# Performance work log

Measured on AMD Instinct MI355X. Metric: run time of the kernel, lower is better.

Reference implementation:

```python
import jax, jax.numpy as jnp
import numpy as np
import math
from jax import lax

STRIDES = (8.0, 16.0, 32.0)
ANCHORS = (
    ((6.1, 8.1), (20.6, 12.6), (11.2, 23.7)),
    ((36.2, 26.8), (25.9, 57.2), (57.8, 47.9)),
    ((122.1, 78.3), (73.7, 143.8), (236.1, 213.1)),
)
NUM_CLASSES = 80
L = NUM_CLASSES + 5
NA = 3
SCORE_T = 0.1
NMS_T = 0.6
DETECTIONS = 100
TOPK = 1000          # static cap on post-threshold candidates per image
IMG = 640            # batched image H=W; also max_size used for class offsets


def setup_inputs() -> dict:
    key = jax.random.key(0)
    ks = jax.random.split(key, 8)
    N = 8
    chans = (128, 256, 512)
    hw = (80, 40, 20)
    inp = {}
    for i, (c, s) in enumerate(zip(chans, hw)):
        inp[f"f{i}"] = jax.random.normal(ks[i], (N, c, s, s), jnp.float32)
        inp[f"w{i}"] = jax.random.normal(ks[3 + i], (NA * L, c), jnp.float32) * 0.02
        b = np.zeros((NA, L), np.float32)
        b[:, 4] += math.log(8 / (416 / STRIDES[i]) ** 2)   # Predictor bias init
        b[:, 5:] += math.log(0.6 / (NUM_CLASSES - 0.99))
        inp[f"b{i}"] = jnp.asarray(b.reshape(-1))
    inp["scale_factors"] = jnp.ones((N,), jnp.float32)
    return inp


def _decode_level(f, w, b, stride, anchors):
    # f: [N,Cin,H,W]; w: [NA*L,Cin]; 1x1 conv == channel GEMM
    N, _, H, W = f.shape
    p = jnp.einsum('nchw,oc->nhwo', f, w) + b
    p = jax.nn.sigmoid(p.reshape(N, H, W, NA, L))
    gx, gy = jnp.meshgrid(jnp.arange(W, dtype=f.dtype), jnp.arange(H, dtype=f.dtype), indexing='xy')
    grid = jnp.stack((gx, gy), axis=-1)                       # [H,W,2] (x,y)
    xy = (2 * p[..., :2] - 0.5 + grid[None, :, :, None, :]) * stride
    wh = 4 * p[..., 2:4] ** 2 * anchors[None, None, None, :, :]
    box = jnp.concatenate((xy, wh), axis=-1).reshape(N, -1, 4)
    obj = p[..., 4].reshape(N, -1)
    cls = p[..., 5:].reshape(N, -1, NUM_CLASSES)
    return box, obj, cls


def _cxcywh2xyxy(b):
    cx, cy, w, h = b[..., 0], b[..., 1], b[..., 2], b[..., 3]
    return jnp.stack((cx - w / 2, cy - h / 2, cx + w / 2, cy + h / 2), axis=-1)


def _iou_one_many(b, boxes):
    lt = jnp.maximum(b[:2], boxes[:, :2])
    rb = jnp.minimum(b[2:], boxes[:, 2:])
    wh = jnp.clip(rb - lt, 0)
    inter = wh[:, 0] * wh[:, 1]
    area_b = (b[2] - b[0]) * (b[3] - b[1])
    areas = (boxes[:, 2] - boxes[:, 0]) * (boxes[:, 3] - boxes[:, 1])
    return inter / (area_b + areas - inter + 1e-7)


def _nms_fixed(boxes, scores):
    # greedy NMS, fixed DETECTIONS iterations; boxes already class-offset
    def step(valid, _):
        s = jnp.where(valid, scores, -jnp.inf)
        i = jnp.argmax(s)
        ok = s[i] > 0.0
        ious = _iou_one_many(boxes[i], boxes)
        nv = valid & (ious <= NMS_T)
        nv = nv.at[i].set(False)
        valid = jnp.where(ok, nv, valid)
        return valid, (jnp.where(ok, i, -1), ok)

    valid0 = scores > SCORE_T
    _, (idx, ok) = lax.scan(step, valid0, None, length=DETECTIONS)
    return idx, ok


def _per_image(boxes, obj, cls, sf):
    scores = obj[:, None] * cls                               # [A,C]
    mask = (obj[:, None] > SCORE_T) & (scores > SCORE_T)
    scores = jnp.where(mask, scores, -1.0)
    topv, topi = lax.top_k(scores.reshape(-1), TOPK)
    anchor = topi // NUM_CLASSES
    label = topi % NUM_CLASSES
    cb = boxes[anchor]
    cb = jnp.clip(cb, 0.0, float(IMG))                        # image_shapes = (IMG, IMG)
    off = cb + (label * IMG).astype(cb.dtype)[:, None]        # batched_nms class offset
    idx, ok = _nms_fixed(off, topv)
    gi = jnp.clip(idx, 0)
    okf = ok.astype(cb.dtype)
    out_box = cb[gi] / sf * okf[:, None]
    out_score = topv[gi] * okf
    out_label = label[gi].astype(cb.dtype) * okf
    return jnp.concatenate((out_box, out_score[:, None], out_label[:, None]), axis=1)  # [DET,6]


def reference(f0, f1, f2, w0, b0, w1, b1, w2, b2, scale_factors):
    feats = (f0, f1, f2)
    ws = (w0, w1, w2)
    bs = (b0, b1, b2)
    boxes, objs, clss = [], [], []
    for i in range(3):
        a = jnp.asarray(ANCHORS[i], dtype=f0.dtype)
        bx, ob, cl = _decode_level(feats[i], ws[i], bs[i], STRIDES[i], a)
        boxes.append(bx)
        objs.append(ob)
        clss.append(cl)
    boxes = _cxcywh2xyxy(jnp.concatenate(boxes, axis=1))      # [N, 25200, 4]
    obj = jnp.concatenate(objs, axis=1)                       # [N, 25200]
    cls = jnp.concatenate(clss, axis=1)                       # [N, 25200, 80]
    return jax.vmap(_per_image)(boxes, obj, cls, scale_factors)  # [N, DET, 6]
```

## Files before the change

kernel.cpp:

```cpp
#include <hip/hip_runtime.h>
#include <math.h>


#define NUM_CLASSES 80
#define IMG_F 640.0f

#define LOGITS_F 0
#define N_LOGITS 48000
#define WPACK_F  48000
#define N_WPACK  3584
#define WT_F     (WPACK_F + N_WPACK)
#define N_WT     344064
#define WT_L0    0
#define WT_L1    49152
#define WT_L2    147456
#define CAND_F   (WT_F + N_WT)
#define CAP1     4096
#define CNT_F    (CAND_F + CAP1*2)
#define IMGBUF_F (CNT_F + 16)
#define CAP2     2048

#define LOGIT_T (-2.1972245773362196f)

__constant__ float d_anch[3][3][2] = {
  {{6.1f,8.1f},{20.6f,12.6f},{11.2f,23.7f}},
  {{36.2f,26.8f},{25.9f,57.2f},{57.8f,47.9f}},
  {{122.1f,78.3f},{73.7f,143.8f},{236.1f,213.1f}},
};
__constant__ float d_stridec[3] = {8.f,16.f,32.f};

__global__ __launch_bounds__(256) void k0_init(
    float* __restrict__ ws, float* __restrict__ out,
    const float* __restrict__ w0, const float* __restrict__ w1,
    const float* __restrict__ w2) {
  int i = blockIdx.x * 256 + threadIdx.x;
  if (i < N_LOGITS) ws[LOGITS_F + i] = 0.f;
  if (i < 4800)     out[i] = 0.f;
  if (i < 16)       ((int*)ws)[CNT_F + i] = 0;
  if (i < N_WPACK) {
    int a = i & 3, c4 = i >> 2;
    float v = 0.f;
    if (a < 3) {
      if (c4 < 128)       v = w0[(a*85+4)*128 + c4];
      else if (c4 < 384)  v = w1[(a*85+4)*256 + (c4-128)];
      else                v = w2[(a*85+4)*512 + (c4-384)];
    }
    ws[WPACK_F + i] = v;
  }
  if (i < N_WT) {
    int level, C, i2;
    const float* w;
    if (i < WT_L1)          { level = 0; C = 128; i2 = i;            w = w0; }
    else if (i < WT_L2)     { level = 1; C = 256; i2 = i - WT_L1;    w = w1; }
    else                    { level = 2; C = 512; i2 = i - WT_L2;    w = w2; }
    int a = i2 / (C * 128);
    int r = i2 - a * (C * 128);
    int c = r >> 7, l = r & 127;
    ws[WT_F + i] = (l < 85) ? w[(size_t)(a * 85 + l) * C + c] : 0.f;
    (void)level;
  }
}

__global__ __launch_bounds__(256) void k1_obj(
    const float* __restrict__ f0, const float* __restrict__ f1,
    const float* __restrict__ f2, const float* __restrict__ b0,
    float* __restrict__ ws) {
  __shared__ float4 wl[128];
  int b = blockIdx.x, tid = threadIdx.x;
  int level, posblk, kc;
  if (b < 200)      { level = 0; posblk = b; kc = 0; }
  else if (b < 400) { int t = b - 200; level = 1; posblk = t % 50; kc = t / 50; }
  else              { int t = b - 400; level = 2; posblk = t % 13; kc = t / 13; }
  const int Cs[3]   = {128, 256, 512};
  const int HWs[3]  = {6400, 1600, 400};
  const int KBs[3]  = {1, 4, 8};
  const int W4B[3]  = {0, 128, 384};
  int C = Cs[level], HW = HWs[level], KB = KBs[level];
  int chunk = C / KB;
  const float* f = (level == 0) ? f0 : (level == 1) ? f1 : f2;
  const float4* wp4 = (const float4*)(ws + WPACK_F);
  int c0 = kc * chunk;
  if (tid < chunk) wl[tid] = wp4[W4B[level] + c0 + tid];
  __syncthreads();
  int pos = posblk * 256 + tid;
  if (pos >= 8 * HW) return;
  int n = pos / HW, s = pos - n * HW;
  const float* fp = f + ((size_t)(n * C + c0)) * HW + s;
  float acc[3] = {0.f, 0.f, 0.f};
  #pragma unroll 16
  for (int c = 0; c < chunk; ++c) {
    float fv = fp[(size_t)c * HW];
    float4 w4 = wl[c];
    acc[0] = fmaf(fv, w4.x, acc[0]);
    acc[1] = fmaf(fv, w4.y, acc[1]);
    acc[2] = fmaf(fv, w4.z, acc[2]);
  }
  if (level == 0) {
    #pragma unroll
    for (int a = 0; a < 3; ++a) {
      float logit = acc[a] + b0[a * 85 + 4];
      if (logit > LOGIT_T) {
        float obj = 1.f / (1.f + expf(-logit));
        int idx = atomicAdd((int*)ws + CNT_F, 1);
        if (idx < CAP1) {
          int* cd = (int*)ws + CAND_F + idx * 2;
          cd[0] = (n << 24) | (0 << 20) | (a << 16) | s;
          ((float*)cd)[1] = obj;
        }
      }
    }
  } else {
    float* lg = ws + LOGITS_F + n * 6000 + ((level == 1) ? 0 : 4800) + s * 3;
    atomicAdd(lg + 0, acc[0]);
    atomicAdd(lg + 1, acc[1]);
    atomicAdd(lg + 2, acc[2]);
  }
}

__global__ __launch_bounds__(256) void k1b_thresh(
    float* __restrict__ ws, const float* __restrict__ b1,
    const float* __restrict__ b2) {
  int i = blockIdx.x * 256 + threadIdx.x;
  if (i >= N_LOGITS) return;
  int n = i / 6000, r = i - n * 6000;
  int level = (r < 4800) ? 1 : 2;
  int roff = (r < 4800) ? r : r - 4800;
  int s = roff / 3, a = roff - s * 3;
  const float* bb = (level == 1) ? b1 : b2;
  float logit = ws[LOGITS_F + i] + bb[a * 85 + 4];
  if (logit > LOGIT_T) {
    float obj = 1.f / (1.f + expf(-logit));
    int idx = atomicAdd((int*)ws + CNT_F, 1);
    if (idx < CAP1) {
      int* cd = (int*)ws + CAND_F + idx * 2;
      cd[0] = (n << 24) | (level << 20) | (a << 16) | s;
      ((float*)cd)[1] = obj;
    }
  }
}

template<int C, int HW, int Wd>
__device__ __forceinline__ void k2_cand(
    int level, int n, int a, int s, float obj,
    const float* __restrict__ f, const float* __restrict__ wTl,
    const float* __restrict__ bb, float* __restrict__ ws,
    float* __restrict__ fc , int lane) {
  #pragma unroll
  for (int j = 0; j < C / 64; ++j)
    fc[lane + 64 * j] = f[((size_t)(n * C + lane + 64 * j)) * HW + s];
  const float* wA = wTl + (size_t)a * C * 128;
  float acc1 = 0.f, acc2 = 0.f;
  #pragma unroll 8
  for (int c = 0; c < C; ++c) {
    float fv = fc[c];
    const float* wl = wA + c * 128;
    acc1 = fmaf(fv, wl[lane], acc1);
    acc2 = fmaf(fv, wl[64 + lane], acc2);
  }
  acc1 += bb[a * 85 + lane];
  float sig1 = 1.f / (1.f + expf(-acc1));
  float sig2 = 0.f;
  if (lane < 21) {
    acc2 += bb[a * 85 + 64 + lane];
    sig2 = 1.f / (1.f + expf(-acc2));
  }
  float p0 = __shfl(sig1, 0, 64), p1 = __shfl(sig1, 1, 64);
  float p2 = __shfl(sig1, 2, 64), p3 = __shfl(sig1, 3, 64);
  int gx = s % Wd, gy = s / Wd;
  float st = d_stridec[level];
  float cx = (2.f * p0 - 0.5f + (float)gx) * st;
  float cy = (2.f * p1 - 0.5f + (float)gy) * st;
  float bw = 4.f * p2 * p2 * d_anch[level][a][0];
  float bh = 4.f * p3 * p3 * d_anch[level][a][1];
  float x1 = fminf(fmaxf(cx - bw * 0.5f, 0.f), IMG_F);
  float y1 = fminf(fmaxf(cy - bh * 0.5f, 0.f), IMG_F);
  float x2 = fminf(fmaxf(cx + bw * 0.5f, 0.f), IMG_F);
  float y2 = fminf(fmaxf(cy + bh * 0.5f, 0.f), IMG_F);
  #pragma unroll
  for (int half = 0; half < 2; ++half) {
    bool on = half == 0 ? (lane >= 5) : (lane < 21);
    float sc = obj * (half == 0 ? sig1 : sig2);
    int cls = half == 0 ? (lane - 5) : (59 + lane);
    if (on && sc > 0.1f) {
      int p = atomicAdd((int*)ws + CNT_F + 1 + n, 1);
      if (p < CAP2) {
        float* dst = ws + IMGBUF_F + ((size_t)(n * CAP2 + p)) * 6;
        dst[0] = x1; dst[1] = y1; dst[2] = x2; dst[3] = y2;
        dst[4] = sc; dst[5] = (float)cls;
      }
    }
  }
}

__global__ __launch_bounds__(256) void k2_score(
    const float* __restrict__ f0, const float* __restrict__ f1,
    const float* __restrict__ f2,
    const float* __restrict__ b0, const float* __restrict__ b1,
    const float* __restrict__ b2, float* __restrict__ ws) {
  __shared__ float fcol[4][512];
  int wv = threadIdx.x >> 6, lane = threadIdx.x & 63;
  int count = min(((int*)ws)[CNT_F], CAP1);
  int nslots = gridDim.x * 4;
  for (int cid = blockIdx.x * 4 + wv; cid < count; cid += nslots) {
    int* cd = (int*)ws + CAND_F + cid * 2;
    int code = cd[0]; float obj = ((float*)cd)[1];
    int n = code >> 24, level = (code >> 20) & 15, a = (code >> 16) & 3, s = code & 0xFFFF;
    if (level == 0)
      k2_cand<128, 6400, 80>(0, n, a, s, obj, f0, ws + WT_F + WT_L0, b0, ws, fcol[wv], lane);
    else if (level == 1)
      k2_cand<256, 1600, 40>(1, n, a, s, obj, f1, ws + WT_F + WT_L1, b1, ws, fcol[wv], lane);
    else
      k2_cand<512, 400, 20>(2, n, a, s, obj, f2, ws + WT_F + WT_L2, b2, ws, fcol[wv], lane);
  }
}

__global__ __launch_bounds__(256) void k3_nms(
    const float* __restrict__ ws, float* __restrict__ out,
    const float* __restrict__ sfp) {
  __shared__ float bx1[CAP2], by1[CAP2], bx2[CAP2], by2[CAP2], bsc[CAP2], blb[CAP2];
  __shared__ int bval[CAP2];
  __shared__ float rs[256];
  __shared__ int ri[256];
  int n = blockIdx.x, tid = threadIdx.x;
  int cnt = min(((const int*)ws)[CNT_F + 1 + n], CAP2);
  for (int i = tid; i < cnt; i += 256) {
    const float* src = ws + IMGBUF_F + ((size_t)(n * CAP2 + i)) * 6;
    bx1[i] = src[0]; by1[i] = src[1]; bx2[i] = src[2]; by2[i] = src[3];
    bsc[i] = src[4]; blb[i] = src[5]; bval[i] = 1;
  }
  __syncthreads();
  float sf = sfp[n];
  for (int it = 0; it < 100; ++it) {
    float best = -1.f; int bi = -1;
    for (int i = tid; i < cnt; i += 256)
      if (bval[i] && bsc[i] > best) { best = bsc[i]; bi = i; }
    rs[tid] = best; ri[tid] = bi;
    __syncthreads();
    for (int off = 128; off > 0; off >>= 1) {
      if (tid < off && rs[tid + off] > rs[tid]) { rs[tid] = rs[tid + off]; ri[tid] = ri[tid + off]; }
      __syncthreads();
    }
    int wi = ri[0]; float wsc = rs[0];
    if (wi < 0) break;
    if (tid == 0) {
      float* o = out + (size_t)(n * 100 + it) * 6;
      o[0] = bx1[wi] / sf; o[1] = by1[wi] / sf;
      o[2] = bx2[wi] / sf; o[3] = by2[wi] / sf;
      o[4] = wsc;          o[5] = blb[wi];
    }
    float ofw = blb[wi] * IMG_F;
    float wx1 = bx1[wi] + ofw, wy1 = by1[wi] + ofw;
    float wx2 = bx2[wi] + ofw, wy2 = by2[wi] + ofw;
    float wa = (wx2 - wx1) * (wy2 - wy1);
    for (int i = tid; i < cnt; i += 256) {
      if (bval[i]) {
        float o2 = blb[i] * IMG_F;
        float x1 = bx1[i] + o2, y1 = by1[i] + o2, x2 = bx2[i] + o2, y2 = by2[i] + o2;
        float iw = fmaxf(fminf(wx2, x2) - fmaxf(wx1, x1), 0.f);
        float ih = fmaxf(fminf(wy2, y2) - fmaxf(wy1, y1), 0.f);
        float inter = iw * ih;
        float area = (x2 - x1) * (y2 - y1);
        float iou = inter / (wa + area - inter + 1e-7f);
        if (iou > 0.6f) bval[i] = 0;
      }
    }
    if (tid == 0) bval[wi] = 0;
    __syncthreads();
  }
}

extern "C" void kernel_launch(void* const* d_in, const int* in_sizes, int n_in,
                              void* d_out, int out_size, void* d_ws, size_t ws_size,
                              hipStream_t stream) {
  const float* f0 = (const float*)d_in[0];
  const float* w0 = (const float*)d_in[1];
  const float* b0 = (const float*)d_in[2];
  const float* f1 = (const float*)d_in[3];
  const float* w1 = (const float*)d_in[4];
  const float* b1 = (const float*)d_in[5];
  const float* f2 = (const float*)d_in[6];
  const float* w2 = (const float*)d_in[7];
  const float* b2 = (const float*)d_in[8];
  const float* sf = (const float*)d_in[9];
  float* out = (float*)d_out;
  float* ws  = (float*)d_ws;

  k0_init   <<<1344, 256, 0, stream>>>(ws, out, w0, w1, w2);
  k1_obj    <<<504, 256, 0, stream>>>(f0, f1, f2, b0, ws);
  k1b_thresh<<<188, 256, 0, stream>>>(ws, b1, b2);
  k2_score  <<<128, 256, 0, stream>>>(f0, f1, f2, b0, b1, b2, ws);
  k3_nms    <<<8, 256, 0, stream>>>(ws, out, sf);
}
```

Baseline: 134.9 us.

## Fuse five kernels into one cooperative kernel with grid-wide syncs

Replaces the five separate launches (init, objectness GEMV, threshold, candidate scoring, NMS) with a single cooperative kernel of 504 blocks that separates the phases with grid.sync(). Shared memory is unioned across phases. The aim is to remove per-launch overhead and inter-kernel gaps. In exchange, the scoring phase now uses 504 blocks instead of 128, the NMS runs on 8 blocks while the rest idle, and each grid barrier has its own cost. Cooperative launch also needs all blocks to be resident at once, which the added launch bounds are meant to ensure.

Measured after the change: 370.0 us. 174% more time.

```diff
diff --git a/kernel.cpp b/kernel.cpp
--- a/kernel.cpp
+++ b/kernel.cpp
@@ -1,5 +1,8 @@
 #include <hip/hip_runtime.h>
+#include <hip/hip_cooperative_groups.h>
 #include <math.h>
+
+namespace cg = cooperative_groups;
 
 
 #define NUM_CLASSES 80
@@ -21,6 +24,7 @@
 #define CAP2     2048
 
 #define LOGIT_T (-2.1972245773362196f)
+#define NBLK 504
 
 __constant__ float d_anch[3][3][2] = {
   {{6.1f,8.1f},{20.6f,12.6f},{11.2f,23.7f}},
@@ -29,122 +33,23 @@
 };
 __constant__ float d_stridec[3] = {8.f,16.f,32.f};
 
-__global__ __launch_bounds__(256) void k0_init(
-    float* __restrict__ ws, float* __restrict__ out,
-    const float* __restrict__ w0, const float* __restrict__ w1,
-    const float* __restrict__ w2) {
-  int i = blockIdx.x * 256 + threadIdx.x;
-  if (i < N_LOGITS) ws[LOGITS_F + i] = 0.f;
-  if (i < 4800)     out[i] = 0.f;
-  if (i < 16)       ((int*)ws)[CNT_F + i] = 0;
-  if (i < N_WPACK) {
-    int a = i & 3, c4 = i >> 2;
-    float v = 0.f;
-    if (a < 3) {
-      if (c4 < 128)       v = w0[(a*85+4)*128 + c4];
-      else if (c4 < 384)  v = w1[(a*85+4)*256 + (c4-128)];
-      else                v = w2[(a*85+4)*512 + (c4-384)];
-    }
-    ws[WPACK_F + i] = v;
-  }
-  if (i < N_WT) {
-    int level, C, i2;
-    const float* w;
-    if (i < WT_L1)          { level = 0; C = 128; i2 = i;            w = w0; }
-    else if (i < WT_L2)     { level = 1; C = 256; i2 = i - WT_L1;    w = w1; }
-    else                    { level = 2; C = 512; i2 = i - WT_L2;    w = w2; }
-    int a = i2 / (C * 128);
-    int r = i2 - a * (C * 128);
-    int c = r >> 7, l = r & 127;
-    ws[WT_F + i] = (l < 85) ? w[(size_t)(a * 85 + l) * C + c] : 0.f;
-    (void)level;
-  }
-}
-
-__global__ __launch_bounds__(256) void k1_obj(
-    const float* __restrict__ f0, const float* __restrict__ f1,
-    const float* __restrict__ f2, const float* __restrict__ b0,
-    float* __restrict__ ws) {
-  __shared__ float4 wl[128];
-  int b = blockIdx.x, tid = threadIdx.x;
-  int level, posblk, kc;
-  if (b < 200)      { level = 0; posblk = b; kc = 0; }
-  else if (b < 400) { int t = b - 200; level = 1; posblk = t % 50; kc = t / 50; }
-  else              { int t = b - 400; level = 2; posblk = t % 13; kc = t / 13; }
-  const int Cs[3]   = {128, 256, 512};
-  const int HWs[3]  = {6400, 1600, 400};
-  const int KBs[3]  = {1, 4, 8};
-  const int W4B[3]  = {0, 128, 384};
-  int C = Cs[level], HW = HWs[level], KB = KBs[level];
-  int chunk = C / KB;
-  const float* f = (level == 0) ? f0 : (level == 1) ? f1 : f2;
-  const float4* wp4 = (const float4*)(ws + WPACK_F);
-  int c0 = kc * chunk;
-  if (tid < chunk) wl[tid] = wp4[W4B[level] + c0 + tid];
-  __syncthreads();
-  int pos = posblk * 256 + tid;
-  if (pos >= 8 * HW) return;
-  int n = pos / HW, s = pos - n * HW;
-  const float* fp = f + ((size_t)(n * C + c0)) * HW + s;
-  float acc[3] = {0.f, 0.f, 0.f};
-  #pragma unroll 16
-  for (int c = 0; c < chunk; ++c) {
-    float fv = fp[(size_t)c * HW];
-    float4 w4 = wl[c];
-    acc[0] = fmaf(fv, w4.x, acc[0]);
-    acc[1] = fmaf(fv, w4.y, acc[1]);
-    acc[2] = fmaf(fv, w4.z, acc[2]);
-  }
-  if (level == 0) {
-    #pragma unroll
-    for (int a = 0; a < 3; ++a) {
-      float logit = acc[a] + b0[a * 85 + 4];
-      if (logit > LOGIT_T) {
-        float obj = 1.f / (1.f + expf(-logit));
-        int idx = atomicAdd((int*)ws + CNT_F, 1);
-        if (idx < CAP1) {
-          int* cd = (int*)ws + CAND_F + idx * 2;
-          cd[0] = (n << 24) | (0 << 20) | (a << 16) | s;
-          ((float*)cd)[1] = obj;
-        }
-      }
-    }
-  } else {
-    float* lg = ws + LOGITS_F + n * 6000 + ((level == 1) ? 0 : 4800) + s * 3;
-    atomicAdd(lg + 0, acc[0]);
-    atomicAdd(lg + 1, acc[1]);
-    atomicAdd(lg + 2, acc[2]);
-  }
-}
-
-__global__ __launch_bounds__(256) void k1b_thresh(
-    float* __restrict__ ws, const float* __restrict__ b1,
-    const float* __restrict__ b2) {
-  int i = blockIdx.x * 256 + threadIdx.x;
-  if (i >= N_LOGITS) return;
-  int n = i / 6000, r = i - n * 6000;
-  int level = (r < 4800) ? 1 : 2;
-  int roff = (r < 4800) ? r : r - 4800;
-  int s = roff / 3, a = roff - s * 3;
-  const float* bb = (level == 1) ? b1 : b2;
-  float logit = ws[LOGITS_F + i] + bb[a * 85 + 4];
-  if (logit > LOGIT_T) {
-    float obj = 1.f / (1.f + expf(-logit));
-    int idx = atomicAdd((int*)ws + CNT_F, 1);
-    if (idx < CAP1) {
-      int* cd = (int*)ws + CAND_F + idx * 2;
-      cd[0] = (n << 24) | (level << 20) | (a << 16) | s;
-      ((float*)cd)[1] = obj;
-    }
-  }
-}
+union ShMem {
+  float4 wl[128];
+  float  fcol[4][512];
+  struct {
+    float bx1[CAP2], by1[CAP2], bx2[CAP2], by2[CAP2], bsc[CAP2], blb[CAP2];
+    int   bval[CAP2];
+    float rs[256];
+    int   ri[256];
+  } nms;
+};
 
 template<int C, int HW, int Wd>
 __device__ __forceinline__ void k2_cand(
     int level, int n, int a, int s, float obj,
     const float* __restrict__ f, const float* __restrict__ wTl,
     const float* __restrict__ bb, float* __restrict__ ws,
-    float* __restrict__ fc , int lane) {
+    float* __restrict__ fc, int lane) {
   #pragma unroll
   for (int j = 0; j < C / 64; ++j)
     fc[lane + 64 * j] = f[((size_t)(n * C + lane + 64 * j)) * HW + s];
@@ -192,80 +97,194 @@
   }
 }
 
-__global__ __launch_bounds__(256) void k2_score(
+__global__ __launch_bounds__(256, 2) void fused_yolo(
     const float* __restrict__ f0, const float* __restrict__ f1,
     const float* __restrict__ f2,
+    const float* __restrict__ w0, const float* __restrict__ w1,
+    const float* __restrict__ w2,
     const float* __restrict__ b0, const float* __restrict__ b1,
-    const float* __restrict__ b2, float* __restrict__ ws) {
-  __shared__ float fcol[4][512];
-  int wv = threadIdx.x >> 6, lane = threadIdx.x & 63;
-  int count = min(((int*)ws)[CNT_F], CAP1);
-  int nslots = gridDim.x * 4;
-  for (int cid = blockIdx.x * 4 + wv; cid < count; cid += nslots) {
-    int* cd = (int*)ws + CAND_F + cid * 2;
-    int code = cd[0]; float obj = ((float*)cd)[1];
-    int n = code >> 24, level = (code >> 20) & 15, a = (code >> 16) & 3, s = code & 0xFFFF;
-    if (level == 0)
-      k2_cand<128, 6400, 80>(0, n, a, s, obj, f0, ws + WT_F + WT_L0, b0, ws, fcol[wv], lane);
-    else if (level == 1)
-      k2_cand<256, 1600, 40>(1, n, a, s, obj, f1, ws + WT_F + WT_L1, b1, ws, fcol[wv], lane);
-    else
-      k2_cand<512, 400, 20>(2, n, a, s, obj, f2, ws + WT_F + WT_L2, b2, ws, fcol[wv], lane);
-  }
-}
-
-__global__ __launch_bounds__(256) void k3_nms(
-    const float* __restrict__ ws, float* __restrict__ out,
-    const float* __restrict__ sfp) {
-  __shared__ float bx1[CAP2], by1[CAP2], bx2[CAP2], by2[CAP2], bsc[CAP2], blb[CAP2];
-  __shared__ int bval[CAP2];
-  __shared__ float rs[256];
-  __shared__ int ri[256];
-  int n = blockIdx.x, tid = threadIdx.x;
-  int cnt = min(((const int*)ws)[CNT_F + 1 + n], CAP2);
-  for (int i = tid; i < cnt; i += 256) {
-    const float* src = ws + IMGBUF_F + ((size_t)(n * CAP2 + i)) * 6;
-    bx1[i] = src[0]; by1[i] = src[1]; bx2[i] = src[2]; by2[i] = src[3];
-    bsc[i] = src[4]; blb[i] = src[5]; bval[i] = 1;
-  }
-  __syncthreads();
-  float sf = sfp[n];
-  for (int it = 0; it < 100; ++it) {
-    float best = -1.f; int bi = -1;
-    for (int i = tid; i < cnt; i += 256)
-      if (bval[i] && bsc[i] > best) { best = bsc[i]; bi = i; }
-    rs[tid] = best; ri[tid] = bi;
+    const float* __restrict__ b2,
+    const float* __restrict__ sfp,
+    float* __restrict__ ws, float* __restrict__ out) {
+  __shared__ ShMem sh;
+  cg::grid_group grid = cg::this_grid();
+  int tid = threadIdx.x;
+  int gsize = NBLK * 256;
+
+  for (int i = blockIdx.x * 256 + tid; i < N_WT; i += gsize) {
+    if (i < N_LOGITS) ws[LOGITS_F + i] = 0.f;
+    if (i < 4800)     out[i] = 0.f;
+    if (i < 16)       ((int*)ws)[CNT_F + i] = 0;
+    if (i < N_WPACK) {
+      int a = i & 3, c4 = i >> 2;
+      float v = 0.f;
+      if (a < 3) {
+        if (c4 < 128)       v = w0[(a*85+4)*128 + c4];
+        else if (c4 < 384)  v = w1[(a*85+4)*256 + (c4-128)];
+        else                v = w2[(a*85+4)*512 + (c4-384)];
+      }
+      ws[WPACK_F + i] = v;
+    }
+    {
+      int C, i2; const float* w;
+      if (i < WT_L1)      { C = 128; i2 = i;         w = w0; }
+      else if (i < WT_L2) { C = 256; i2 = i - WT_L1; w = w1; }
+      else                { C = 512; i2 = i - WT_L2; w = w2; }
+      int a = i2 / (C * 128);
+      int r = i2 - a * (C * 128);
+      int c = r >> 7, l = r & 127;
+      ws[WT_F + i] = (l < 85) ? w[(size_t)(a * 85 + l) * C + c] : 0.f;
+    }
+  }
+  grid.sync();
+
+  {
+    int b = blockIdx.x;
+    int level, posblk, kc;
+    if (b < 200)      { level = 0; posblk = b; kc = 0; }
+    else if (b < 400) { int t = b - 200; level = 1; posblk = t % 50; kc = t / 50; }
+    else              { int t = b - 400; level = 2; posblk = t % 13; kc = t / 13; }
+    const int Cs[3]   = {128, 256, 512};
+    const int HWs[3]  = {6400, 1600, 400};
+    const int KBs[3]  = {1, 4, 8};
+    const int W4B[3]  = {0, 128, 384};
+    int C = Cs[level], HW = HWs[level], KB = KBs[level];
+    int chunk = C / KB;
+    const float* f = (level == 0) ? f0 : (level == 1) ? f1 : f2;
+    const float4* wp4 = (const float4*)(ws + WPACK_F);
+    int c0 = kc * chunk;
+    if (tid < chunk) sh.wl[tid] = wp4[W4B[level] + c0 + tid];
     __syncthreads();
-    for (int off = 128; off > 0; off >>= 1) {
-      if (tid < off && rs[tid + off] > rs[tid]) { rs[tid] = rs[tid + off]; ri[tid] = ri[tid + off]; }
+    int pos = posblk * 256 + tid;
+    if (pos < 8 * HW) {
+      int n = pos / HW, s = pos - n * HW;
+      const float* fp = f + ((size_t)(n * C + c0)) * HW + s;
+      float acc[3] = {0.f, 0.f, 0.f};
+      #pragma unroll 16
+      for (int c = 0; c < chunk; ++c) {
+        float fv = fp[(size_t)c * HW];
+        float4 w4 = sh.wl[c];
+        acc[0] = fmaf(fv, w4.x, acc[0]);
+        acc[1] = fmaf(fv, w4.y, acc[1]);
+        acc[2] = fmaf(fv, w4.z, acc[2]);
+      }
+      if (level == 0) {
+        #pragma unroll
+        for (int a = 0; a < 3; ++a) {
+          float logit = acc[a] + b0[a * 85 + 4];
+          if (logit > LOGIT_T) {
+            float obj = 1.f / (1.f + expf(-logit));
+            int idx = atomicAdd((int*)ws + CNT_F, 1);
+            if (idx < CAP1) {
+              int* cd = (int*)ws + CAND_F + idx * 2;
+              cd[0] = (n << 24) | (0 << 20) | (a << 16) | s;
+              ((float*)cd)[1] = obj;
+            }
+          }
+        }
+      } else {
+        float* lg = ws + LOGITS_F + n * 6000 + ((level == 1) ? 0 : 4800) + s * 3;
+        atomicAdd(lg + 0, acc[0]);
+        atomicAdd(lg + 1, acc[1]);
+        atomicAdd(lg + 2, acc[2]);
+      }
+    }
+  }
+  grid.sync();
+
+  {
+    int i = blockIdx.x * 256 + tid;
+    if (i < N_LOGITS) {
+      int n = i / 6000, r = i - n * 6000;
+      int level = (r < 4800) ? 1 : 2;
+      int roff = (r < 4800) ? r : r - 4800;
+      int s = roff / 3, a = roff - s * 3;
+      const float* bb = (level == 1) ? b1 : b2;
+      float logit = ws[LOGITS_F + i] + bb[a * 85 + 4];
+      if (logit > LOGIT_T) {
+        float obj = 1.f / (1.f + expf(-logit));
+        int idx = atomicAdd((int*)ws + CNT_F, 1);
+        if (idx < CAP1) {
+          int* cd = (int*)ws + CAND_F + idx * 2;
+          cd[0] = (n << 24) | (level << 20) | (a << 16) | s;
+          ((float*)cd)[1] = obj;
+        }
+      }
+    }
+  }
+  grid.sync();
+
+  {
+    int wv = tid >> 6, lane = tid & 63;
+    int count = min(((int*)ws)[CNT_F], CAP1);
+    int nslots = NBLK * 4;
+    for (int cid = blockIdx.x * 4 + wv; cid < count; cid += nslots) {
+      int* cd = (int*)ws + CAND_F + cid * 2;
+      int code = cd[0]; float obj = ((float*)cd)[1];
+      int n = code >> 24, level = (code >> 20) & 15, a = (code >> 16) & 3, s = code & 0xFFFF;
+      if (level == 0)
+        k2_cand<128, 6400, 80>(0, n, a, s, obj, f0, ws + WT_F + WT_L0, b0, ws, sh.fcol[wv], lane);
+      else if (level == 1)
+        k2_cand<256, 1600, 40>(1, n, a, s, obj, f1, ws + WT_F + WT_L1, b1, ws, sh.fcol[wv], lane);
+      else
+        k2_cand<512, 400, 20>(2, n, a, s, obj, f2, ws + WT_F + WT_L2, b2, ws, sh.fcol[wv], lane);
+    }
+  }
+  grid.sync();
+
+  if (blockIdx.x < 8) {
+    int n = blockIdx.x;
+    int cnt = min(((const int*)ws)[CNT_F + 1 + n], CAP2);
+    for (int i = tid; i < cnt; i += 256) {
+      const float* src = ws + IMGBUF_F + ((size_t)(n * CAP2 + i)) * 6;
+      sh.nms.bx1[i] = src[0]; sh.nms.by1[i] = src[1];
+      sh.nms.bx2[i] = src[2]; sh.nms.by2[i] = src[3];
+      sh.nms.bsc[i] = src[4]; sh.nms.blb[i] = src[5];
+      sh.nms.bval[i] = 1;
+    }
+    __syncthreads();
+    float sf = sfp[n];
+    for (int it = 0; it < 100; ++it) {
+      float best = -1.f; int bi = -1;
+      for (int i = tid; i < cnt; i += 256)
+        if (sh.nms.bval[i] && sh.nms.bsc[i] > best) { best = sh.nms.bsc[i]; bi = i; }
+      sh.nms.rs[tid] = best; sh.nms.ri[tid] = bi;
       __syncthreads();
-    }
-    int wi = ri[0]; float wsc = rs[0];
-    if (wi < 0) break;
-    if (tid == 0) {
-      float* o = out + (size_t)(n * 100 + it) * 6;
-      o[0] = bx1[wi] / sf; o[1] = by1[wi] / sf;
-      o[2] = bx2[wi] / sf; o[3] = by2[wi] / sf;
-      o[4] = wsc;          o[5] = blb[wi];
-    }
-    float ofw = blb[wi] * IMG_F;
-    float wx1 = bx1[wi] + ofw, wy1 = by1[wi] + ofw;
-    float wx2 = bx2[wi] + ofw, wy2 = by2[wi] + ofw;
-    float wa = (wx2 - wx1) * (wy2 - wy1);
-    for (int i = tid; i < cnt; i += 256) {
-      if (bval[i]) {
-        float o2 = blb[i] * IMG_F;
-        float x1 = bx1[i] + o2, y1 = by1[i] + o2, x2 = bx2[i] + o2, y2 = by2[i] + o2;
-        float iw = fmaxf(fminf(wx2, x2) - fmaxf(wx1, x1), 0.f);
-        float ih = fmaxf(fminf(wy2, y2) - fmaxf(wy1, y1), 0.f);
-        float inter = iw * ih;
-        float area = (x2 - x1) * (y2 - y1);
-        float iou = inter / (wa + area - inter + 1e-7f);
-        if (iou > 0.6f) bval[i] = 0;
-      }
-    }
-    if (tid == 0) bval[wi] = 0;
-    __syncthreads();
+      for (int off = 128; off > 0; off >>= 1) {
+        if (tid < off && sh.nms.rs[tid + off] > sh.nms.rs[tid]) {
+          sh.nms.rs[tid] = sh.nms.rs[tid + off];
+          sh.nms.ri[tid] = sh.nms.ri[tid + off];
+        }
+        __syncthreads();
+      }
+      int wi = sh.nms.ri[0]; float wsc = sh.nms.rs[0];
+      if (wi < 0) break;
+      if (tid == 0) {
+        float* o = out + (size_t)(n * 100 + it) * 6;
+        o[0] = sh.nms.bx1[wi] / sf; o[1] = sh.nms.by1[wi] / sf;
+        o[2] = sh.nms.bx2[wi] / sf; o[3] = sh.nms.by2[wi] / sf;
+        o[4] = wsc;                 o[5] = sh.nms.blb[wi];
+      }
+      float ofw = sh.nms.blb[wi] * IMG_F;
+      float wx1 = sh.nms.bx1[wi] + ofw, wy1 = sh.nms.by1[wi] + ofw;
+      float wx2 = sh.nms.bx2[wi] + ofw, wy2 = sh.nms.by2[wi] + ofw;
+      float wa = (wx2 - wx1) * (wy2 - wy1);
+      for (int i = tid; i < cnt; i += 256) {
+        if (sh.nms.bval[i]) {
+          float o2 = sh.nms.blb[i] * IMG_F;
+          float x1 = sh.nms.bx1[i] + o2, y1 = sh.nms.by1[i] + o2;
+          float x2 = sh.nms.bx2[i] + o2, y2 = sh.nms.by2[i] + o2;
+          float iw = fmaxf(fminf(wx2, x2) - fmaxf(wx1, x1), 0.f);
+          float ih = fmaxf(fminf(wy2, y2) - fmaxf(wy1, y1), 0.f);
+          float inter = iw * ih;
+          float area = (x2 - x1) * (y2 - y1);
+          float iou = inter / (wa + area - inter + 1e-7f);
+          if (iou > 0.6f) sh.nms.bval[i] = 0;
+        }
+      }
+      if (tid == 0) sh.nms.bval[wi] = 0;
+      __syncthreads();
+    }
   }
 }
 
@@ -285,9 +304,12 @@
   float* out = (float*)d_out;
   float* ws  = (float*)d_ws;
 
-  k0_init   <<<1344, 256, 0, stream>>>(ws, out, w0, w1, w2);
-  k1_obj    <<<504, 256, 0, stream>>>(f0, f1, f2, b0, ws);
-  k1b_thresh<<<188, 256, 0, stream>>>(ws, b1, b2);
-  k2_score  <<<128, 256, 0, stream>>>(f0, f1, f2, b0, b1, b2, ws);
-  k3_nms    <<<8, 256, 0, stream>>>(ws, out, sf);
+  void* kargs[] = {
+    (void*)&f0, (void*)&f1, (void*)&f2,
+    (void*)&w0, (void*)&w1, (void*)&w2,
+    (void*)&b0, (void*)&b1, (void*)&b2,
+    (void*)&sf, (void*)&ws, (void*)&out,
+  };
+  hipLaunchCooperativeKernel((const void*)fused_yolo, dim3(NBLK), dim3(256),
+                             kargs, 0, stream);
 }
```

## Replace atomic split-K objectness pass with in-block shared-memory reduction

Applied to the files above, without the earlier changes.

The objectness 1x1-conv pass now has each thread process four spatial positions with float4 loads over a 16-channel slice. Partial sums are reduced in shared memory inside the block instead of through global float atomics. This removes the logits zero-init, the packed objectness-weight staging, and the separate threshold kernel, so one fewer launch runs. Weights are read directly from global memory, and the larger block count with a serial per-output reduction loop adds some in-block work.

Result: faster. 128.7 us (-4.6%).

```diff
diff --git a/kernel.cpp b/kernel.cpp
--- a/kernel.cpp
+++ b/kernel.cpp
@@ -2,19 +2,14 @@
 #include <math.h>
 
 
-#define NUM_CLASSES 80
 #define IMG_F 640.0f
 
-#define LOGITS_F 0
-#define N_LOGITS 48000
-#define WPACK_F  48000
-#define N_WPACK  3584
-#define WT_F     (WPACK_F + N_WPACK)
+#define WT_F     0
 #define N_WT     344064
 #define WT_L0    0
 #define WT_L1    49152
 #define WT_L2    147456
-#define CAND_F   (WT_F + N_WT)
+#define CAND_F   344064
 #define CAP1     4096
 #define CNT_F    (CAND_F + CAP1*2)
 #define IMGBUF_F (CNT_F + 16)
@@ -29,122 +24,96 @@
 };
 __constant__ float d_stridec[3] = {8.f,16.f,32.f};
 
-__global__ __launch_bounds__(256) void k0_init(
+__global__ __launch_bounds__(256) void ka_init(
     float* __restrict__ ws, float* __restrict__ out,
     const float* __restrict__ w0, const float* __restrict__ w1,
     const float* __restrict__ w2) {
   int i = blockIdx.x * 256 + threadIdx.x;
-  if (i < N_LOGITS) ws[LOGITS_F + i] = 0.f;
-  if (i < 4800)     out[i] = 0.f;
-  if (i < 16)       ((int*)ws)[CNT_F + i] = 0;
-  if (i < N_WPACK) {
-    int a = i & 3, c4 = i >> 2;
-    float v = 0.f;
-    if (a < 3) {
-      if (c4 < 128)       v = w0[(a*85+4)*128 + c4];
-      else if (c4 < 384)  v = w1[(a*85+4)*256 + (c4-128)];
-      else                v = w2[(a*85+4)*512 + (c4-384)];
-    }
-    ws[WPACK_F + i] = v;
-  }
+  if (i < 4800) out[i] = 0.f;
+  if (i < 16)   ((int*)ws)[CNT_F + i] = 0;
   if (i < N_WT) {
-    int level, C, i2;
-    const float* w;
-    if (i < WT_L1)          { level = 0; C = 128; i2 = i;            w = w0; }
-    else if (i < WT_L2)     { level = 1; C = 256; i2 = i - WT_L1;    w = w1; }
-    else                    { level = 2; C = 512; i2 = i - WT_L2;    w = w2; }
+    int C, i2; const float* w;
+    if (i < WT_L1)      { C = 128; i2 = i;         w = w0; }
+    else if (i < WT_L2) { C = 256; i2 = i - WT_L1; w = w1; }
+    else                { C = 512; i2 = i - WT_L2; w = w2; }
     int a = i2 / (C * 128);
     int r = i2 - a * (C * 128);
     int c = r >> 7, l = r & 127;
     ws[WT_F + i] = (l < 85) ? w[(size_t)(a * 85 + l) * C + c] : 0.f;
-    (void)level;
-  }
-}
-
-__global__ __launch_bounds__(256) void k1_obj(
+  }
+}
+
+__global__ __launch_bounds__(256) void kb_obj(
     const float* __restrict__ f0, const float* __restrict__ f1,
-    const float* __restrict__ f2, const float* __restrict__ b0,
-    float* __restrict__ ws) {
-  __shared__ float4 wl[128];
-  int b = blockIdx.x, tid = threadIdx.x;
-  int level, posblk, kc;
-  if (b < 200)      { level = 0; posblk = b; kc = 0; }
-  else if (b < 400) { int t = b - 200; level = 1; posblk = t % 50; kc = t / 50; }
-  else              { int t = b - 400; level = 2; posblk = t % 13; kc = t / 13; }
-  const int Cs[3]   = {128, 256, 512};
-  const int HWs[3]  = {6400, 1600, 400};
-  const int KBs[3]  = {1, 4, 8};
-  const int W4B[3]  = {0, 128, 384};
-  int C = Cs[level], HW = HWs[level], KB = KBs[level];
-  int chunk = C / KB;
-  const float* f = (level == 0) ? f0 : (level == 1) ? f1 : f2;
-  const float4* wp4 = (const float4*)(ws + WPACK_F);
-  int c0 = kc * chunk;
-  if (tid < chunk) wl[tid] = wp4[W4B[level] + c0 + tid];
+    const float* __restrict__ f2,
+    const float* __restrict__ w0, const float* __restrict__ w1,
+    const float* __restrict__ w2,
+    const float* __restrict__ b0, const float* __restrict__ b1,
+    const float* __restrict__ b2, float* __restrict__ ws) {
+  __shared__ float red[3104];
+  int b = blockIdx.x, t = threadIdx.x;
+  int level, Q, lq, S, bq0, C, HW;
+  const float *f, *w, *bb;
+  if (b < 400)      { level = 0; Q = 32; lq = 5; S = 8;  bq0 = b * 32;         C = 128; HW = 6400; f = f0; w = w0; bb = b0; }
+  else if (b < 600) { level = 1; Q = 16; lq = 4; S = 16; bq0 = (b - 400) * 16; C = 256; HW = 1600; f = f1; w = w1; bb = b1; }
+  else              { level = 2; Q = 8;  lq = 3; S = 32; bq0 = (b - 600) * 8;  C = 512; HW = 400;  f = f2; w = w2; bb = b2; }
+  int q = t & (Q - 1), sl = t >> lq;
+  int qpi = HW >> 2;
+  int gq = bq0 + q;
+  int n = gq / qpi;
+  int sq = (gq - n * qpi) << 2;
+  int kbase = sl * 16;
+  const float* fp = f + ((size_t)(n * C + kbase)) * HW + sq;
+  const float* wp = w + 4 * C + kbase;
+  float acc[3][4] = {{0.f,0.f,0.f,0.f},{0.f,0.f,0.f,0.f},{0.f,0.f,0.f,0.f}};
+  #pragma unroll
+  for (int c = 0; c < 16; ++c) {
+    float4 v = *(const float4*)(fp + (size_t)c * HW);
+    float wa0 = wp[c];
+    float wa1 = wp[85 * C + c];
+    float wa2 = wp[170 * C + c];
+    acc[0][0] = fmaf(v.x, wa0, acc[0][0]); acc[0][1] = fmaf(v.y, wa0, acc[0][1]);
+    acc[0][2] = fmaf(v.z, wa0, acc[0][2]); acc[0][3] = fmaf(v.w, wa0, acc[0][3]);
+    acc[1][0] = fmaf(v.x, wa1, acc[1][0]); acc[1][1] = fmaf(v.y, wa1, acc[1][1]);
+    acc[1][2] = fmaf(v.z, wa1, acc[1][2]); acc[1][3] = fmaf(v.w, wa1, acc[1][3]);
+    acc[2][0] = fmaf(v.x, wa2, acc[2][0]); acc[2][1] = fmaf(v.y, wa2, acc[2][1]);
+    acc[2][2] = fmaf(v.z, wa2, acc[2][2]); acc[2][3] = fmaf(v.w, wa2, acc[2][3]);
+  }
+  int stride = Q * 12 + 1;
+  int base = sl * stride + q * 12;
+  #pragma unroll
+  for (int a = 0; a < 3; ++a)
+    #pragma unroll
+    for (int p = 0; p < 4; ++p)
+      red[base + a * 4 + p] = acc[a][p];
   __syncthreads();
-  int pos = posblk * 256 + tid;
-  if (pos >= 8 * HW) return;
-  int n = pos / HW, s = pos - n * HW;
-  const float* fp = f + ((size_t)(n * C + c0)) * HW + s;
-  float acc[3] = {0.f, 0.f, 0.f};
-  #pragma unroll 16
-  for (int c = 0; c < chunk; ++c) {
-    float fv = fp[(size_t)c * HW];
-    float4 w4 = wl[c];
-    acc[0] = fmaf(fv, w4.x, acc[0]);
-    acc[1] = fmaf(fv, w4.y, acc[1]);
-    acc[2] = fmaf(fv, w4.z, acc[2]);
-  }
-  if (level == 0) {
-    #pragma unroll
-    for (int a = 0; a < 3; ++a) {
-      float logit = acc[a] + b0[a * 85 + 4];
-      if (logit > LOGIT_T) {
-        float obj = 1.f / (1.f + expf(-logit));
-        int idx = atomicAdd((int*)ws + CNT_F, 1);
-        if (idx < CAP1) {
-          int* cd = (int*)ws + CAND_F + idx * 2;
-          cd[0] = (n << 24) | (0 << 20) | (a << 16) | s;
-          ((float*)cd)[1] = obj;
-        }
+  for (int r = t; r < Q * 12; r += 256) {
+    int qq = r / 12, ap = r - qq * 12;
+    int a = ap >> 2, p = ap & 3;
+    float sum = 0.f;
+    for (int s2 = 0; s2 < S; ++s2) sum += red[s2 * stride + qq * 12 + ap];
+    float logit = sum + bb[a * 85 + 4];
+    if (logit > LOGIT_T) {
+      float obj = 1.f / (1.f + expf(-logit));
+      int gq2 = bq0 + qq;
+      int n2 = gq2 / qpi;
+      int s = ((gq2 - n2 * qpi) << 2) + p;
+      int idx = atomicAdd((int*)ws + CNT_F, 1);
+      if (idx < CAP1) {
+        int* cd = (int*)ws + CAND_F + idx * 2;
+        cd[0] = (n2 << 24) | (level << 20) | (a << 16) | s;
+        ((float*)cd)[1] = obj;
       }
     }
-  } else {
-    float* lg = ws + LOGITS_F + n * 6000 + ((level == 1) ? 0 : 4800) + s * 3;
-    atomicAdd(lg + 0, acc[0]);
-    atomicAdd(lg + 1, acc[1]);
-    atomicAdd(lg + 2, acc[2]);
-  }
-}
-
-__global__ __launch_bounds__(256) void k1b_thresh(
-    float* __restrict__ ws, const float* __restrict__ b1,
-    const float* __restrict__ b2) {
-  int i = blockIdx.x * 256 + threadIdx.x;
-  if (i >= N_LOGITS) return;
-  int n = i / 6000, r = i - n * 6000;
-  int level = (r < 4800) ? 1 : 2;
-  int roff = (r < 4800) ? r : r - 4800;
-  int s = roff / 3, a = roff - s * 3;
-  const float* bb = (level == 1) ? b1 : b2;
-  float logit = ws[LOGITS_F + i] + bb[a * 85 + 4];
-  if (logit > LOGIT_T) {
-    float obj = 1.f / (1.f + expf(-logit));
-    int idx = atomicAdd((int*)ws + CNT_F, 1);
-    if (idx < CAP1) {
-      int* cd = (int*)ws + CAND_F + idx * 2;
-      cd[0] = (n << 24) | (level << 20) | (a << 16) | s;
-      ((float*)cd)[1] = obj;
-    }
   }
 }
 
 template<int C, int HW, int Wd>
-__device__ __forceinline__ void k2_cand(
+__device__ __forceinline__ void kc_cand(
     int level, int n, int a, int s, float obj,
     const float* __restrict__ f, const float* __restrict__ wTl,
     const float* __restrict__ bb, float* __restrict__ ws,
-    float* __restrict__ fc , int lane) {
+    float* __restrict__ fc, int lane) {
   #pragma unroll
   for (int j = 0; j < C / 64; ++j)
     fc[lane + 64 * j] = f[((size_t)(n * C + lane + 64 * j)) * HW + s];
@@ -192,7 +161,7 @@
   }
 }
 
-__global__ __launch_bounds__(256) void k2_score(
+__global__ __launch_bounds__(256) void kc_score(
     const float* __restrict__ f0, const float* __restrict__ f1,
     const float* __restrict__ f2,
     const float* __restrict__ b0, const float* __restrict__ b1,
@@ -206,15 +175,15 @@
     int code = cd[0]; float obj = ((float*)cd)[1];
     int n = code >> 24, level = (code >> 20) & 15, a = (code >> 16) & 3, s = code & 0xFFFF;
     if (level == 0)
-      k2_cand<128, 6400, 80>(0, n, a, s, obj, f0, ws + WT_F + WT_L0, b0, ws, fcol[wv], lane);
+      kc_cand<128, 6400, 80>(0, n, a, s, obj, f0, ws + WT_F + WT_L0, b0, ws, fcol[wv], lane);
     else if (level == 1)
-      k2_cand<256, 1600, 40>(1, n, a, s, obj, f1, ws + WT_F + WT_L1, b1, ws, fcol[wv], lane);
+      kc_cand<256, 1600, 40>(1, n, a, s, obj, f1, ws + WT_F + WT_L1, b1, ws, fcol[wv], lane);
     else
-      k2_cand<512, 400, 20>(2, n, a, s, obj, f2, ws + WT_F + WT_L2, b2, ws, fcol[wv], lane);
-  }
-}
-
-__global__ __launch_bounds__(256) void k3_nms(
+      kc_cand<512, 400, 20>(2, n, a, s, obj, f2, ws + WT_F + WT_L2, b2, ws, fcol[wv], lane);
+  }
+}
+
+__global__ __launch_bounds__(256) void kd_nms(
     const float* __restrict__ ws, float* __restrict__ out,
     const float* __restrict__ sfp) {
   __shared__ float bx1[CAP2], by1[CAP2], bx2[CAP2], by2[CAP2], bsc[CAP2], blb[CAP2];
@@ -285,9 +254,8 @@
   float* out = (float*)d_out;
   float* ws  = (float*)d_ws;
 
-  k0_init   <<<1344, 256, 0, stream>>>(ws, out, w0, w1, w2);
-  k1_obj    <<<504, 256, 0, stream>>>(f0, f1, f2, b0, ws);
-  k1b_thresh<<<188, 256, 0, stream>>>(ws, b1, b2);
-  k2_score  <<<128, 256, 0, stream>>>(f0, f1, f2, b0, b1, b2, ws);
-  k3_nms    <<<8, 256, 0, stream>>>(ws, out, sf);
-}
+  ka_init <<<1344, 256, 0, stream>>>(ws, out, w0, w1, w2);
+  kb_obj  <<<700,  256, 0, stream>>>(f0, f1, f2, w0, w1, w2, b0, b1, b2, ws);
+  kc_score<<<128,  256, 0, stream>>>(f0, f1, f2, b0, b1, b2, ws);
+  kd_nms  <<<8,    256, 0, stream>>>(ws, out, sf);
+}
```
